# Performance work log

Measured on AMD Instinct MI355X. Metric: run time of the kernel, lower is better.

The kernel has to match this reference:

```python
import math
import jax, jax.numpy as jnp
import numpy as np

B, T, D_IN, D_SAE, K = 256, 64, 512, 4096, 32

def _sinusoidal_posemb(T, d):
    pos = jnp.arange(T, dtype=jnp.float32)[:, None]
    div = jnp.exp(jnp.arange(0, d, 2, dtype=jnp.float32) * (-(math.log(10000.0) / d)))
    pe = jnp.zeros((T, d), dtype=jnp.float32)
    pe = pe.at[:, 0::2].set(jnp.sin(pos * div))
    pe = pe.at[:, 1::2].set(jnp.cos(pos * div))
    return pe

def setup_inputs() -> dict:
    key = jax.random.key(0)
    k0, k1, k2 = jax.random.split(key, 3)
    x = jax.random.normal(k0, (B, T, D_IN), dtype=jnp.float32)
    W_enc = jax.random.normal(k1, (D_IN, D_SAE), dtype=jnp.float32) / D_IN ** 0.5
    W_dec = jax.random.normal(k2, (D_SAE, T, D_IN), dtype=jnp.float32) / D_SAE ** 0.5
    b_enc = jnp.zeros((D_SAE,), dtype=jnp.float32)
    b_dec = jnp.zeros((T, D_IN), dtype=jnp.float32)
    return {"x": x, "W_enc": W_enc, "W_dec": W_dec, "b_enc": b_enc, "b_dec": b_dec}

def reference(x, W_enc, W_dec, b_enc, b_dec):
    pe = _sinusoidal_posemb(T, D_IN)              # (T, d_in) buffer
    x_plus = x + pe[None]                         # (B, T, d_in)
    pre = jnp.einsum('btd,ds->bs', x_plus, W_enc) + b_enc  # (B, d_sae)
    v, i = jax.lax.top_k(pre, K)                  # (B, K) each
    rows = jnp.arange(B)[:, None]
    z = jnp.zeros_like(pre).at[rows, i].set(jax.nn.relu(v))  # sparse scatter
    x_hat = jnp.einsum('bs,std->btd', z, W_dec) + b_dec      # (B, T, d_in)
    loss = jnp.mean(jnp.sum((x_hat - x) ** 2, axis=-1))
    return loss, x_hat, z
```

## Files before the change

### kernel.cpp

```cpp
#include <hip/hip_runtime.h>
#include <math.h>

#define NB 256
#define NT 64
#define DIN 512
#define DSAE 4096
#define NK 32

typedef float f32x4 __attribute__((ext_vector_type(4)));

__global__ __launch_bounds__(512) void k_xs(const float* __restrict__ x,
                                            float* __restrict__ xs,
                                            float* __restrict__ out) {
    const int b = blockIdx.x, d = threadIdx.x;
    if (b == 0 && d == 0) out[0] = 0.f;
    int j = d >> 1;
    float freq = expf((float)(2 * j) * (-9.210340371976184f / 512.0f));
    float pes = 0.f;
    if (d & 1) {
        for (int t = 0; t < NT; ++t) pes += cosf((float)t * freq);
    } else {
        for (int t = 0; t < NT; ++t) pes += sinf((float)t * freq);
    }
    const float* xp = x + (size_t)b * NT * DIN + d;
    float acc = 0.f;
#pragma unroll 16
    for (int t = 0; t < NT; ++t) acc += xp[(size_t)t * DIN];
    xs[(size_t)b * DIN + d] = acc + pes;
}

__global__ __launch_bounds__(256) void k_pre(const float* __restrict__ xs,
                                             const float* __restrict__ W,
                                             const float* __restrict__ b_enc,
                                             float* __restrict__ pre) {
    __shared__ float xs_t[DIN][8];
    const int tid = threadIdx.x;
    const int s = blockIdx.x * 256 + tid;
    const int b0 = blockIdx.y * 8;
    for (int i = tid; i < 8 * DIN; i += 256) {
        int bb = i >> 9, d = i & 511;
        xs_t[d][bb] = xs[(size_t)(b0 + bb) * DIN + d];
    }
    __syncthreads();
    float a0=0,a1=0,a2=0,a3=0,a4=0,a5=0,a6=0,a7=0;
    float c0=0,c1=0,c2=0,c3=0,c4=0,c5=0,c6=0,c7=0;
    const float* wp = W + s;
#pragma unroll 4
    for (int d = 0; d < DIN; d += 2) {
        float w0 = wp[(size_t)d * DSAE];
        float w1 = wp[(size_t)(d + 1) * DSAE];
        float4 lo0 = *(const float4*)&xs_t[d][0];
        float4 hi0 = *(const float4*)&xs_t[d][4];
        float4 lo1 = *(const float4*)&xs_t[d + 1][0];
        float4 hi1 = *(const float4*)&xs_t[d + 1][4];
        a0 += lo0.x * w0; a1 += lo0.y * w0; a2 += lo0.z * w0; a3 += lo0.w * w0;
        a4 += hi0.x * w0; a5 += hi0.y * w0; a6 += hi0.z * w0; a7 += hi0.w * w0;
        c0 += lo1.x * w1; c1 += lo1.y * w1; c2 += lo1.z * w1; c3 += lo1.w * w1;
        c4 += hi1.x * w1; c5 += hi1.y * w1; c6 += hi1.z * w1; c7 += hi1.w * w1;
    }
    float be = b_enc[s];
    pre[(size_t)(b0 + 0) * DSAE + s] = a0 + c0 + be;
    pre[(size_t)(b0 + 1) * DSAE + s] = a1 + c1 + be;
    pre[(size_t)(b0 + 2) * DSAE + s] = a2 + c2 + be;
    pre[(size_t)(b0 + 3) * DSAE + s] = a3 + c3 + be;
    pre[(size_t)(b0 + 4) * DSAE + s] = a4 + c4 + be;
    pre[(size_t)(b0 + 5) * DSAE + s] = a5 + c5 + be;
    pre[(size_t)(b0 + 6) * DSAE + s] = a6 + c6 + be;
    pre[(size_t)(b0 + 7) * DSAE + s] = a7 + c7 + be;
}

__global__ __launch_bounds__(64) void k_topk(const float* __restrict__ pre,
                                             float* __restrict__ z_out,
                                             int* __restrict__ idx_s,
                                             float* __restrict__ zv_s) {
    const int b = blockIdx.x, lane = threadIdx.x;
    const float* pr = pre + (size_t)b * DSAE;
    float* zr = z_out + (size_t)b * DSAE;
    __shared__ float lv[64 * 65];
    __shared__ float lgv[64 * 8];
    __shared__ int   lga[64 * 8];
    for (int j = lane; j < DSAE; j += 64) __builtin_nontemporal_store(0.f, &zr[j]);
    const int base = lane * 65;
    float v[64];
#pragma unroll
    for (int j = 0; j < 64; ++j) v[j] = pr[j * 64 + lane];
#pragma unroll
    for (int j = 0; j < 64; ++j) lv[base + j] = v[j];
    float lmax = -INFINITY; int larg = 0;
#pragma unroll
    for (int g = 0; g < 8; ++g) {
        float m = v[g * 8]; int a = g * 8;
#pragma unroll
        for (int t = 1; t < 8; ++t)
            if (v[g * 8 + t] > m) { m = v[g * 8 + t]; a = g * 8 + t; }
        lgv[lane * 8 + g] = m; lga[lane * 8 + g] = a;
        if (m > lmax) { lmax = m; larg = a; }
    }
    __syncthreads();
    int myi = 0; float myv = 0.f;
    for (int k = 0; k < NK; ++k) {
        float bv = lmax; int be = larg * 64 + lane;
#pragma unroll
        for (int off = 32; off >= 1; off >>= 1) {
            float ov = __shfl_down(bv, off);
            int oe = __shfl_down(be, off);
            if (ov > bv || (ov == bv && oe < be)) { bv = ov; be = oe; }
        }
        bv = __shfl(bv, 0); be = __shfl(be, 0);
        if (lane == k) { myi = be; myv = bv > 0.f ? bv : 0.f; }
        if (lane == (be & 63)) {
            int j0 = be >> 6;
            lv[base + j0] = -INFINITY;
            int g0 = j0 >> 3;
            float m = -INFINITY; int a2 = g0 << 3;
            for (int t = 0; t < 8; ++t) {
                float x2 = lv[base + (g0 << 3) + t];
                if (x2 > m) { m = x2; a2 = (g0 << 3) + t; }
            }
            lgv[lane * 8 + g0] = m; lga[lane * 8 + g0] = a2;
            lmax = -INFINITY; larg = 0;
            for (int g = 0; g < 8; ++g) {
                float x2 = lgv[lane * 8 + g];
                if (x2 > lmax) { lmax = x2; larg = lga[lane * 8 + g]; }
            }
        }
    }
    int rank = 0;
#pragma unroll
    for (int j = 0; j < NK; ++j) {
        int oi = __shfl(myi, j);
        if (lane < NK && oi < myi) rank++;
    }
    if (lane < NK) {
        idx_s[b * NK + rank] = myi;
        zv_s[b * NK + rank] = myv;
        __builtin_nontemporal_store(myv, &zr[myi]);
    }
}

__global__ __launch_bounds__(256) void k_dec(const float* __restrict__ x,
                                             const float* __restrict__ Wd,
                                             const float* __restrict__ bd,
                                             const int* __restrict__ idx_s,
                                             const float* __restrict__ zv_s,
                                             float* __restrict__ out) {
    const int b = blockIdx.y, chunk = blockIdx.x, tid = threadIdx.x;
    __shared__ int si[NK];
    __shared__ float sz[NK];
    if (tid < NK) { si[tid] = idx_s[b * NK + tid]; sz[tid] = zv_s[b * NK + tid]; }
    __syncthreads();
    const int f0 = chunk * 1024 + tid;
    const float4* bd4 = (const float4*)bd;
    float4 acc0 = bd4[f0];
    float4 acc1 = bd4[f0 + 256];
    float4 acc2 = bd4[f0 + 512];
    float4 acc3 = bd4[f0 + 768];
    for (int k = 0; k < NK; ++k) {
        const float4* w4 = (const float4*)(Wd + (size_t)si[k] * (NT * DIN));
        float zk = sz[k];
        float4 w0 = w4[f0], w1 = w4[f0 + 256], w2 = w4[f0 + 512], w3 = w4[f0 + 768];
        acc0.x += zk * w0.x; acc0.y += zk * w0.y; acc0.z += zk * w0.z; acc0.w += zk * w0.w;
        acc1.x += zk * w1.x; acc1.y += zk * w1.y; acc1.z += zk * w1.z; acc1.w += zk * w1.w;
        acc2.x += zk * w2.x; acc2.y += zk * w2.y; acc2.z += zk * w2.z; acc2.w += zk * w2.w;
        acc3.x += zk * w3.x; acc3.y += zk * w3.y; acc3.z += zk * w3.z; acc3.w += zk * w3.w;
    }
    const f32x4* xr4 = (const f32x4*)(x + (size_t)b * (NT * DIN));
    float* xh = out + 1 + (size_t)b * (NT * DIN);
    float lsum = 0.f;
    {
        f32x4 xv = __builtin_nontemporal_load(&xr4[f0]);
        float d0 = acc0.x - xv.x, d1 = acc0.y - xv.y, d2 = acc0.z - xv.z, d3 = acc0.w - xv.w;
        lsum += d0 * d0; lsum += d1 * d1; lsum += d2 * d2; lsum += d3 * d3;
        int e = f0 * 4;
        __builtin_nontemporal_store(acc0.x, &xh[e]);   __builtin_nontemporal_store(acc0.y, &xh[e+1]);
        __builtin_nontemporal_store(acc0.z, &xh[e+2]); __builtin_nontemporal_store(acc0.w, &xh[e+3]);
    }
    {
        f32x4 xv = __builtin_nontemporal_load(&xr4[f0 + 256]);
        float d0 = acc1.x - xv.x, d1 = acc1.y - xv.y, d2 = acc1.z - xv.z, d3 = acc1.w - xv.w;
        lsum += d0 * d0; lsum += d1 * d1; lsum += d2 * d2; lsum += d3 * d3;
        int e = (f0 + 256) * 4;
        __builtin_nontemporal_store(acc1.x, &xh[e]);   __builtin_nontemporal_store(acc1.y, &xh[e+1]);
        __builtin_nontemporal_store(acc1.z, &xh[e+2]); __builtin_nontemporal_store(acc1.w, &xh[e+3]);
    }
    {
        f32x4 xv = __builtin_nontemporal_load(&xr4[f0 + 512]);
        float d0 = acc2.x - xv.x, d1 = acc2.y - xv.y, d2 = acc2.z - xv.z, d3 = acc2.w - xv.w;
        lsum += d0 * d0; lsum += d1 * d1; lsum += d2 * d2; lsum += d3 * d3;
        int e = (f0 + 512) * 4;
        __builtin_nontemporal_store(acc2.x, &xh[e]);   __builtin_nontemporal_store(acc2.y, &xh[e+1]);
        __builtin_nontemporal_store(acc2.z, &xh[e+2]); __builtin_nontemporal_store(acc2.w, &xh[e+3]);
    }
    {
        f32x4 xv = __builtin_nontemporal_load(&xr4[f0 + 768]);
        float d0 = acc3.x - xv.x, d1 = acc3.y - xv.y, d2 = acc3.z - xv.z, d3 = acc3.w - xv.w;
        lsum += d0 * d0; lsum += d1 * d1; lsum += d2 * d2; lsum += d3 * d3;
        int e = (f0 + 768) * 4;
        __builtin_nontemporal_store(acc3.x, &xh[e]);   __builtin_nontemporal_store(acc3.y, &xh[e+1]);
        __builtin_nontemporal_store(acc3.z, &xh[e+2]); __builtin_nontemporal_store(acc3.w, &xh[e+3]);
    }

#pragma unroll
    for (int off = 32; off >= 1; off >>= 1) lsum += __shfl_down(lsum, off);
    __shared__ float red[4];
    if ((tid & 63) == 0) red[tid >> 6] = lsum;
    __syncthreads();
    if (tid == 0) {
        float tot = red[0] + red[1] + red[2] + red[3];
        atomicAdd(out, tot * (1.0f / (NB * NT)));
    }
}

extern "C" void kernel_launch(void* const* d_in, const int* in_sizes, int n_in,
                              void* d_out, int out_size, void* d_ws, size_t ws_size,
                              hipStream_t stream) {
    const float* x     = (const float*)d_in[0];
    const float* W_enc = (const float*)d_in[1];
    const float* W_dec = (const float*)d_in[2];
    const float* b_enc = (const float*)d_in[3];
    const float* b_dec = (const float*)d_in[4];
    float* out = (float*)d_out;

    float* ws    = (float*)d_ws;
    float* xs    = ws;
    float* pre   = ws + 131072;
    int*   idx_s = (int*)(ws + 1179648);
    float* zv_s  = ws + 1187840;

    float* z_out = out + 1 + (size_t)NB * NT * DIN;

    k_xs<<<NB, 512, 0, stream>>>(x, xs, out);
    k_pre<<<dim3(16, 32), 256, 0, stream>>>(xs, W_enc, b_enc, pre);
    k_topk<<<NB, 64, 0, stream>>>(pre, z_out, idx_s, zv_s);
    k_dec<<<dim3(8, NB), 256, 0, stream>>>(x, W_dec, b_dec, idx_s, zv_s, out);
}
```

Baseline: 139.8 us.

## Split decoder into two passes over halves of the feature dictionary

The decoder kernel becomes two launches. The first accumulates contributions from sparse features with index below 2048 and writes partial x_hat. The second reloads that partial, adds features with index 2048 and above, and computes the loss. The aim is to limit the W_dec working set each pass touches (half of the 512 MB) so it can get more L2/MALL reuse across batches. The cost is an extra write and read of the full x_hat and an extra kernel launch.

Result: slower. 157.1 us (+12.4%).

```diff
diff --git a/kernel.cpp b/kernel.cpp
--- a/kernel.cpp
+++ b/kernel.cpp
@@ -6,6 +6,7 @@
 #define DIN 512
 #define DSAE 4096
 #define NK 32
+#define HALF 2048
 
 typedef float f32x4 __attribute__((ext_vector_type(4)));
 
@@ -138,6 +139,7 @@
     }
 }
 
+template<int PASS>
 __global__ __launch_bounds__(256) void k_dec(const float* __restrict__ x,
                                              const float* __restrict__ Wd,
                                              const float* __restrict__ bd,
@@ -150,64 +152,73 @@
     if (tid < NK) { si[tid] = idx_s[b * NK + tid]; sz[tid] = zv_s[b * NK + tid]; }
     __syncthreads();
     const int f0 = chunk * 1024 + tid;
-    const float4* bd4 = (const float4*)bd;
-    float4 acc0 = bd4[f0];
-    float4 acc1 = bd4[f0 + 256];
-    float4 acc2 = bd4[f0 + 512];
-    float4 acc3 = bd4[f0 + 768];
+    float* xh = out + 1 + (size_t)b * (NT * DIN);
+
+    float acc[16];
+    if (PASS == 0) {
+        const float4* bd4 = (const float4*)bd;
+#pragma unroll
+        for (int q = 0; q < 4; ++q) {
+            float4 v = bd4[f0 + q * 256];
+            acc[q*4+0] = v.x; acc[q*4+1] = v.y; acc[q*4+2] = v.z; acc[q*4+3] = v.w;
+        }
+    } else {
+#pragma unroll
+        for (int q = 0; q < 4; ++q) {
+            int e = (f0 + q * 256) * 4;
+            acc[q*4+0] = __builtin_nontemporal_load(&xh[e]);
+            acc[q*4+1] = __builtin_nontemporal_load(&xh[e+1]);
+            acc[q*4+2] = __builtin_nontemporal_load(&xh[e+2]);
+            acc[q*4+3] = __builtin_nontemporal_load(&xh[e+3]);
+        }
+    }
+
     for (int k = 0; k < NK; ++k) {
-        const float4* w4 = (const float4*)(Wd + (size_t)si[k] * (NT * DIN));
+        int s = si[k];
+        if (PASS == 0) { if (s >= HALF) break; }
+        else           { if (s <  HALF) continue; }
+        const float4* w4 = (const float4*)(Wd + (size_t)s * (NT * DIN));
         float zk = sz[k];
         float4 w0 = w4[f0], w1 = w4[f0 + 256], w2 = w4[f0 + 512], w3 = w4[f0 + 768];
-        acc0.x += zk * w0.x; acc0.y += zk * w0.y; acc0.z += zk * w0.z; acc0.w += zk * w0.w;
-        acc1.x += zk * w1.x; acc1.y += zk * w1.y; acc1.z += zk * w1.z; acc1.w += zk * w1.w;
-        acc2.x += zk * w2.x; acc2.y += zk * w2.y; acc2.z += zk * w2.z; acc2.w += zk * w2.w;
-        acc3.x += zk * w3.x; acc3.y += zk * w3.y; acc3.z += zk * w3.z; acc3.w += zk * w3.w;
-    }
-    const f32x4* xr4 = (const f32x4*)(x + (size_t)b * (NT * DIN));
-    float* xh = out + 1 + (size_t)b * (NT * DIN);
-    float lsum = 0.f;
-    {
-        f32x4 xv = __builtin_nontemporal_load(&xr4[f0]);
-        float d0 = acc0.x - xv.x, d1 = acc0.y - xv.y, d2 = acc0.z - xv.z, d3 = acc0.w - xv.w;
-        lsum += d0 * d0; lsum += d1 * d1; lsum += d2 * d2; lsum += d3 * d3;
-        int e = f0 * 4;
-        __builtin_nontemporal_store(acc0.x, &xh[e]);   __builtin_nontemporal_store(acc0.y, &xh[e+1]);
-        __builtin_nontemporal_store(acc0.z, &xh[e+2]); __builtin_nontemporal_store(acc0.w, &xh[e+3]);
-    }
-    {
-        f32x4 xv = __builtin_nontemporal_load(&xr4[f0 + 256]);
-        float d0 = acc1.x - xv.x, d1 = acc1.y - xv.y, d2 = acc1.z - xv.z, d3 = acc1.w - xv.w;
-        lsum += d0 * d0; lsum += d1 * d1; lsum += d2 * d2; lsum += d3 * d3;
-        int e = (f0 + 256) * 4;
-        __builtin_nontemporal_store(acc1.x, &xh[e]);   __builtin_nontemporal_store(acc1.y, &xh[e+1]);
-        __builtin_nontemporal_store(acc1.z, &xh[e+2]); __builtin_nontemporal_store(acc1.w, &xh[e+3]);
-    }
-    {
-        f32x4 xv = __builtin_nontemporal_load(&xr4[f0 + 512]);
-        float d0 = acc2.x - xv.x, d1 = acc2.y - xv.y, d2 = acc2.z - xv.z, d3 = acc2.w - xv.w;
-        lsum += d0 * d0; lsum += d1 * d1; lsum += d2 * d2; lsum += d3 * d3;
-        int e = (f0 + 512) * 4;
-        __builtin_nontemporal_store(acc2.x, &xh[e]);   __builtin_nontemporal_store(acc2.y, &xh[e+1]);
-        __builtin_nontemporal_store(acc2.z, &xh[e+2]); __builtin_nontemporal_store(acc2.w, &xh[e+3]);
-    }
-    {
-        f32x4 xv = __builtin_nontemporal_load(&xr4[f0 + 768]);
-        float d0 = acc3.x - xv.x, d1 = acc3.y - xv.y, d2 = acc3.z - xv.z, d3 = acc3.w - xv.w;
-        lsum += d0 * d0; lsum += d1 * d1; lsum += d2 * d2; lsum += d3 * d3;
-        int e = (f0 + 768) * 4;
-        __builtin_nontemporal_store(acc3.x, &xh[e]);   __builtin_nontemporal_store(acc3.y, &xh[e+1]);
-        __builtin_nontemporal_store(acc3.z, &xh[e+2]); __builtin_nontemporal_store(acc3.w, &xh[e+3]);
-    }
-
-#pragma unroll
-    for (int off = 32; off >= 1; off >>= 1) lsum += __shfl_down(lsum, off);
-    __shared__ float red[4];
-    if ((tid & 63) == 0) red[tid >> 6] = lsum;
-    __syncthreads();
-    if (tid == 0) {
-        float tot = red[0] + red[1] + red[2] + red[3];
-        atomicAdd(out, tot * (1.0f / (NB * NT)));
+        acc[0]  += zk * w0.x; acc[1]  += zk * w0.y; acc[2]  += zk * w0.z; acc[3]  += zk * w0.w;
+        acc[4]  += zk * w1.x; acc[5]  += zk * w1.y; acc[6]  += zk * w1.z; acc[7]  += zk * w1.w;
+        acc[8]  += zk * w2.x; acc[9]  += zk * w2.y; acc[10] += zk * w2.z; acc[11] += zk * w2.w;
+        acc[12] += zk * w3.x; acc[13] += zk * w3.y; acc[14] += zk * w3.z; acc[15] += zk * w3.w;
+    }
+
+    if (PASS == 0) {
+#pragma unroll
+        for (int q = 0; q < 4; ++q) {
+            int e = (f0 + q * 256) * 4;
+            __builtin_nontemporal_store(acc[q*4+0], &xh[e]);
+            __builtin_nontemporal_store(acc[q*4+1], &xh[e+1]);
+            __builtin_nontemporal_store(acc[q*4+2], &xh[e+2]);
+            __builtin_nontemporal_store(acc[q*4+3], &xh[e+3]);
+        }
+    } else {
+        const f32x4* xr4 = (const f32x4*)(x + (size_t)b * (NT * DIN));
+        float lsum = 0.f;
+#pragma unroll
+        for (int q = 0; q < 4; ++q) {
+            f32x4 xv = __builtin_nontemporal_load(&xr4[f0 + q * 256]);
+            float d0 = acc[q*4+0] - xv.x, d1 = acc[q*4+1] - xv.y;
+            float d2 = acc[q*4+2] - xv.z, d3 = acc[q*4+3] - xv.w;
+            lsum += d0 * d0; lsum += d1 * d1; lsum += d2 * d2; lsum += d3 * d3;
+            int e = (f0 + q * 256) * 4;
+            __builtin_nontemporal_store(acc[q*4+0], &xh[e]);
+            __builtin_nontemporal_store(acc[q*4+1], &xh[e+1]);
+            __builtin_nontemporal_store(acc[q*4+2], &xh[e+2]);
+            __builtin_nontemporal_store(acc[q*4+3], &xh[e+3]);
+        }
+#pragma unroll
+        for (int off = 32; off >= 1; off >>= 1) lsum += __shfl_down(lsum, off);
+        __shared__ float red[4];
+        if ((tid & 63) == 0) red[tid >> 6] = lsum;
+        __syncthreads();
+        if (tid == 0) {
+            float tot = red[0] + red[1] + red[2] + red[3];
+            atomicAdd(out, tot * (1.0f / (NB * NT)));
+        }
     }
 }
 
@@ -232,5 +243,6 @@
     k_xs<<<NB, 512, 0, stream>>>(x, xs, out);
     k_pre<<<dim3(16, 32), 256, 0, stream>>>(xs, W_enc, b_enc, pre);
     k_topk<<<NB, 64, 0, stream>>>(pre, z_out, idx_s, zv_s);
-    k_dec<<<dim3(8, NB), 256, 0, stream>>>(x, W_dec, b_dec, idx_s, zv_s, out);
-}
+    k_dec<0><<<dim3(8, NB), 256, 0, stream>>>(x, W_dec, b_dec, idx_s, zv_s, out);
+    k_dec<1><<<dim3(8, NB), 256, 0, stream>>>(x, W_dec, b_dec, idx_s, zv_s, out);
+}
```
